# Performance work log

Hardware: AMD Instinct MI355X
Metric: run time of the kernel (lower is better)

Reference implementation:

```python
import jax, jax.numpy as jnp
import numpy as np

N = 200000  # num nodes == num edges (edge_weight serves as both node feature and edge weight)
D_HID = 128
D_OUT = 2


def setup_inputs() -> dict:
    key = jax.random.key(0)
    ks = jax.random.split(key, 5)
    edge_index = jax.random.randint(ks[0], (2, N), 0, N, dtype=jnp.int64)
    edge_weight = jax.random.uniform(ks[1], (N,), dtype=jnp.float32)
    # Glorot-ish init for GCNConv linear layers (bias=True by default in PyG)
    W1 = jax.random.normal(ks[2], (1, D_HID), dtype=jnp.float32) * (1.0 / np.sqrt(1))
    W2 = jax.random.normal(ks[3], (D_HID, D_HID), dtype=jnp.float32) * (1.0 / np.sqrt(D_HID))
    W3 = jax.random.normal(ks[4], (D_HID, D_OUT), dtype=jnp.float32) * (1.0 / np.sqrt(D_HID))
    b1 = jnp.zeros((D_HID,), dtype=jnp.float32)
    b2 = jnp.zeros((D_HID,), dtype=jnp.float32)
    b3 = jnp.zeros((D_OUT,), dtype=jnp.float32)
    return {"edge_index": edge_index, "edge_weight": edge_weight,
            "W1": W1, "b1": b1, "W2": W2, "b2": b2, "W3": W3, "b3": b3}


def reference(edge_index, edge_weight, W1, b1, W2, b2, W3, b3):
    n = edge_weight.shape[0]
    src, dst = edge_index[0], edge_index[1]
    # GCN symmetric normalization with self-loops (PyG gcn_norm, fill_value=1.0)
    loops = jnp.arange(n)
    src_f = jnp.concatenate([src, loops])            # [2N]
    dst_f = jnp.concatenate([dst, loops])            # [2N]
    w_f = jnp.concatenate([edge_weight, jnp.ones((n,), edge_weight.dtype)])
    deg = jax.ops.segment_sum(w_f, dst_f, num_segments=n)
    dinv = jnp.where(deg > 0, deg ** -0.5, 0.0)
    norm = dinv[src_f] * w_f * dinv[dst_f]           # [2N], identical for all layers

    def conv(x, W, b):
        h = x @ W                                    # linear transform first (out <= in path)
        msg = h[src_f] * norm[:, None]               # gather + edge scale
        return jax.ops.segment_sum(msg, dst_f, num_segments=n) + b  # scatter-add aggregate

    x = edge_weight[:, None]                         # node features = edge weights, [N,1]
    x = jax.nn.relu(conv(x, W1, b1))
    x = jax.nn.relu(conv(x, W2, b2))
    x = jax.nn.relu(conv(x, W3, b3))
    return jax.nn.log_softmax(x, axis=1)
```

## Files before the change

kernel.cpp:

```cpp
#include <hip/hip_runtime.h>

#define NN 200000
#define NE 200000
#define DH 128
#define CAP 16

typedef float f32x4 __attribute__((ext_vector_type(4)));
typedef _Float16 f16x8 __attribute__((ext_vector_type(8)));
#define AS1 __attribute__((address_space(1)))
#define AS3 __attribute__((address_space(3)))

__device__ __forceinline__ unsigned pack2h(float a, float b) {
  unsigned short ua = __builtin_bit_cast(unsigned short, (_Float16)a);
  unsigned short ub = __builtin_bit_cast(unsigned short, (_Float16)b);
  return (unsigned)ua | ((unsigned)ub << 16);
}
__device__ __forceinline__ float deg_of(int p) {
  return (float)(((unsigned)p) & 0x03FFFFFFu) * (1.0f / 1048576.0f) + 1.0f;
}
__device__ __forceinline__ int cnt_of(int p) { return (int)(((unsigned)p) >> 26); }

__global__ void k_build(const int* __restrict__ src, const int* __restrict__ dst,
                        const float* __restrict__ ew, int* __restrict__ pdeg,
                        int2* __restrict__ slot,
                        const float* __restrict__ W2, unsigned* __restrict__ w2g) {
  int tid = threadIdx.x;
  int e = blockIdx.x * 256 + tid;
  if (e < NE) {
    int d = dst[e];
    int sv = src[e];
    float w = ew[e];
    int addend = __float2int_rn(w * 1048576.0f) | (1 << 26);
    int old = atomicAdd(&pdeg[d], addend);
    int r = (int)(((unsigned)old) >> 26);
    if (r < CAP) slot[d * CAP + r] = make_int2(sv, __float_as_int(w));
  }
  if (blockIdx.x < 32) {
    int gid = blockIdx.x * 256 + tid;
    int fkc = gid >> 8, l = (gid >> 2) & 63, dd = gid & 3;
    int n = (fkc >> 2) * 16 + (l & 15);
    int dwp = (fkc & 3) * 16 + (l >> 4) * 4 + dd;
    w2g[gid] = pack2h(W2[(2 * dwp) * DH + n], W2[(2 * dwp + 1) * DH + n]);
  }
}

__global__ void k_nodes(const float* __restrict__ ew, const int* __restrict__ pdeg,
                        int2* __restrict__ slot, float* __restrict__ s) {
  int d = blockIdx.x * 256 + threadIdx.x;
  if (d >= NN) return;
  int p = pdeg[d];
  float dv = rsqrtf(deg_of(p));
  int cnt = min(cnt_of(p), CAP);
  float acc = 0.f;
  for (int j0 = 0; j0 < cnt; j0 += 4) {
    int2 sl[4];
    int sidx[4];
    bool v[4];
#pragma unroll
    for (int u = 0; u < 4; u++) {
      v[u] = (j0 + u) < cnt;
      sl[u] = slot[d * CAP + min(j0 + u, CAP - 1)];
      sidx[u] = v[u] ? sl[u].x : d;
    }
    float dg[4], we[4];
#pragma unroll
    for (int u = 0; u < 4; u++) { dg[u] = deg_of(pdeg[sidx[u]]); we[u] = ew[sidx[u]]; }
#pragma unroll
    for (int u = 0; u < 4; u++) {
      if (v[u]) {
        float wdvs = __int_as_float(sl[u].y) * rsqrtf(dg[u]);
        acc = fmaf(wdvs, we[u], acc);
        slot[d * CAP + j0 + u] = make_int2(sl[u].x, __float_as_int(wdvs * dv));
      }
    }
  }
  s[d] = dv * fmaf(dv, ew[d], acc);
}

__global__ __launch_bounds__(256, 3) void k_layer2(
    const float* __restrict__ s, const int* __restrict__ pdeg,
    const int2* __restrict__ slot,
    const float* __restrict__ W1, const float* __restrict__ b1,
    const float* __restrict__ b2, const float* __restrict__ W3,
    const unsigned* __restrict__ w2g, float* __restrict__ h3) {
  __shared__ __align__(16) char smem[49152];
  unsigned* w2t = (unsigned*)smem;
  uint4* tAf = (uint4*)(smem + 32768);
  float* eS = (float*)(smem + 32768);
  float* eN = (float*)(smem + 32768 + 4352);
  int tid = threadIdx.x;
  int wv = tid >> 6;

#pragma unroll
  for (int i = 0; i < 8; ++i)
    __builtin_amdgcn_global_load_lds(
        (const AS1 unsigned*)(w2g + i * 1024 + tid * 4),
        (AS3 unsigned*)(w2t + i * 1024 + wv * 256), 16, 0, 0);

  int base = blockIdx.x * 64;
  int lr15 = tid & 15, q = (tid >> 4) & 3;
  int d = base + wv * 16 + lr15;
  int myn = wv * 16 + lr15;

  int2 sl4[4];
#pragma unroll
  for (int it = 0; it < 4; ++it) sl4[it] = slot[base * CAP + it * 256 + tid];

  float w1r[32], b1r[32];
#pragma unroll
  for (int c = 0; c < 32; c++) { w1r[c] = W1[q * 32 + c]; b1r[c] = b1[q * 32 + c]; }
  int pd = pdeg[d];
  float sd = s[d];
  float dvd = rsqrtf(deg_of(pd));
  float sn = dvd * dvd;
  int mycnt = min(cnt_of(pd), CAP);

#pragma unroll
  for (int it = 0; it < 4; ++it) {
    int idx = it * 256 + tid;
    int nl = idx >> 4, j = idx & 15;
    if ((unsigned)sl4[it].x < NN) {
      eS[nl * 17 + j] = s[sl4[it].x];
      eN[nl * 17 + j] = __int_as_float(sl4[it].y);
    }
  }

  float acc[32];
#pragma unroll
  for (int c = 0; c < 32; c++)
    acc[c] = sn * fmaxf(fmaf(sd, w1r[c], b1r[c]), 0.f);
  __syncthreads();

  for (int j = 0; j < mycnt; ++j) {
    float ss = eS[myn * 17 + j], nr = eN[myn * 17 + j];
#pragma unroll
    for (int c = 0; c < 32; c++)
      acc[c] = fmaf(nr, fmaxf(fmaf(ss, w1r[c], b1r[c]), 0.f), acc[c]);
  }
  __syncthreads();

#pragma unroll
  for (int hi = 0; hi < 4; ++hi) {
    uint4 u;
    u.x = pack2h(acc[8 * hi + 0], acc[8 * hi + 1]);
    u.y = pack2h(acc[8 * hi + 2], acc[8 * hi + 3]);
    u.z = pack2h(acc[8 * hi + 4], acc[8 * hi + 5]);
    u.w = pack2h(acc[8 * hi + 6], acc[8 * hi + 7]);
    tAf[(wv * 4 + q) * 64 + hi * 16 + lr15] = u;
  }
  __syncthreads();

  int l = tid & 63, g = l >> 4, lr = l & 15;
  f32x4 acc8[8];
#pragma unroll
  for (int f = 0; f < 8; f++) acc8[f] = (f32x4){0.f, 0.f, 0.f, 0.f};
#pragma unroll
  for (int kc = 0; kc < 4; kc++) {
    f16x8 av = __builtin_bit_cast(f16x8, tAf[(wv * 4 + kc) * 64 + l]);
#pragma unroll
    for (int f = 0; f < 8; f++) {
      f16x8 bv = __builtin_bit_cast(f16x8, *(const uint4*)(w2t + ((f * 4 + kc) * 64 + l) * 4));
      acc8[f] = __builtin_amdgcn_mfma_f32_16x16x32_f16(av, bv, acc8[f], 0, 0, 0);
    }
  }

  float p0[4] = {0.f, 0.f, 0.f, 0.f}, p1[4] = {0.f, 0.f, 0.f, 0.f};
#pragma unroll
  for (int f = 0; f < 8; f++) {
    int n = f * 16 + lr;
    float bb = b2[n];
    float2 w3v = ((const float2*)W3)[n];
#pragma unroll
    for (int r = 0; r < 4; r++) {
      float v = fmaxf(acc8[f][r] + bb, 0.f);
      p0[r] = fmaf(v, w3v.x, p0[r]);
      p1[r] = fmaf(v, w3v.y, p1[r]);
    }
  }
#pragma unroll
  for (int r = 0; r < 4; r++) {
#pragma unroll
    for (int m = 8; m; m >>= 1) {
      p0[r] += __shfl_xor(p0[r], m);
      p1[r] += __shfl_xor(p1[r], m);
    }
  }
  if (lr == 0) {
#pragma unroll
    for (int r = 0; r < 4; r++) {
      int node = base + wv * 16 + g * 4 + r;
      ((float2*)h3)[node] = make_float2(p0[r], p1[r]);
    }
  }
}

__global__ void k_final(const float* __restrict__ h3, const int* __restrict__ pdeg,
                        const int2* __restrict__ slot, const float* __restrict__ b3,
                        float* __restrict__ out) {
  int d = blockIdx.x * 256 + threadIdx.x;
  if (d >= NN) return;
  int p = pdeg[d];
  float dvd = rsqrtf(deg_of(p));
  float sn = dvd * dvd;
  int cnt = min(cnt_of(p), CAP);
  float2 hv = ((const float2*)h3)[d];
  float y0 = sn * hv.x, y1 = sn * hv.y;
  for (int j0 = 0; j0 < cnt; j0 += 4) {
    int2 sl[4];
    int idx4[4];
    bool v[4];
#pragma unroll
    for (int u = 0; u < 4; u++) {
      v[u] = (j0 + u) < cnt;
      sl[u] = slot[d * CAP + min(j0 + u, CAP - 1)];
      idx4[u] = v[u] ? sl[u].x : d;
    }
    float2 hs[4];
#pragma unroll
    for (int u = 0; u < 4; u++) hs[u] = ((const float2*)h3)[idx4[u]];
#pragma unroll
    for (int u = 0; u < 4; u++) {
      if (v[u]) {
        float nr = __int_as_float(sl[u].y);
        y0 = fmaf(nr, hs[u].x, y0);
        y1 = fmaf(nr, hs[u].y, y1);
      }
    }
  }
  float z0 = fmaxf(y0 + b3[0], 0.f);
  float z1 = fmaxf(y1 + b3[1], 0.f);
  float m = fmaxf(z0, z1);
  float lse = m + logf(expf(z0 - m) + expf(z1 - m));
  out[2 * d] = z0 - lse;
  out[2 * d + 1] = z1 - lse;
}

extern "C" void kernel_launch(void* const* d_in, const int* in_sizes, int n_in,
                              void* d_out, int out_size, void* d_ws, size_t ws_size,
                              hipStream_t stream) {
  const int* ei = (const int*)d_in[0];
  const int* srcp = ei;
  const int* dstp = ei + NE;
  const float* ew = (const float*)d_in[1];
  const float* W1 = (const float*)d_in[2];
  const float* b1 = (const float*)d_in[3];
  const float* W2 = (const float*)d_in[4];
  const float* b2 = (const float*)d_in[5];
  const float* W3 = (const float*)d_in[6];
  const float* b3 = (const float*)d_in[7];
  float* out = (float*)d_out;

  char* ws = (char*)d_ws;
  size_t off = 0;
  auto alloc = [&](size_t bytes) -> void* {
    void* p = ws + off;
    off = (off + bytes + 255) & ~size_t(255);
    return p;
  };
  int* pdeg = (int*)alloc(NN * 4);
  size_t zero_bytes = off;
  int2* slot = (int2*)alloc((size_t)NN * CAP * 8);
  float* s = (float*)alloc(NN * 4);
  unsigned* w2g = (unsigned*)alloc(8192 * 4);
  float* h3 = (float*)alloc(NN * 2 * 4);
  (void)ws_size; (void)in_sizes; (void)n_in; (void)out_size;

  const int nbE = (NE + 255) / 256;
  const int nbN = (NN + 255) / 256;

  hipMemsetAsync(pdeg, 0, zero_bytes, stream);
  k_build<<<nbE, 256, 0, stream>>>(srcp, dstp, ew, pdeg, slot, W2, w2g);
  k_nodes<<<nbN, 256, 0, stream>>>(ew, pdeg, slot, s);
  k_layer2<<<NN / 64, 256, 0, stream>>>(s, pdeg, slot, W1, b1, b2, W3, w2g, h3);
  k_final<<<nbN, 256, 0, stream>>>(h3, pdeg, slot, b3, out);
}
```

Baseline: 132.1 us.

## Process two tiles per layer2 block and specialize neighbor loops for low degree

k_layer2 now runs half as many blocks, and each block handles two 64-node tiles. This amortizes the 32KB W2 LDS load and the W1/b1 register setup. The LDS neighbor staging is cut to 12 slots per node, and neighbors beyond 12 fall back to direct global loads. k_nodes and k_final load the first four slots with two 16-byte vector loads and handle the remaining neighbors in a scalar loop, avoiding the old padded min-clamped batch of four. The cost is fewer resident blocks in layer2, which gives less parallelism and latency hiding, plus extra syncs between tiles.

```diff
diff --git a/kernel.cpp b/kernel.cpp
--- a/kernel.cpp
+++ b/kernel.cpp
@@ -4,6 +4,8 @@
 #define NE 200000
 #define DH 128
 #define CAP 16
+#define NTILES (NN / 64)
+#define L2BLK ((NTILES + 1) / 2)
 
 typedef float f32x4 __attribute__((ext_vector_type(4)));
 typedef _Float16 f16x8 __attribute__((ext_vector_type(8)));
@@ -51,28 +53,31 @@
   int p = pdeg[d];
   float dv = rsqrtf(deg_of(p));
   int cnt = min(cnt_of(p), CAP);
+  const int4* sp = (const int4*)(slot + d * CAP);
+  int4 a = sp[0], b = sp[1];
+  int2 sl[4] = {{a.x, a.y}, {a.z, a.w}, {b.x, b.y}, {b.z, b.w}};
+  int n4 = min(cnt, 4);
+  int sidx[4];
+  bool v[4];
+#pragma unroll
+  for (int u = 0; u < 4; u++) { v[u] = u < n4; sidx[u] = v[u] ? sl[u].x : d; }
+  float dg[4], we[4];
+#pragma unroll
+  for (int u = 0; u < 4; u++) { dg[u] = deg_of(pdeg[sidx[u]]); we[u] = ew[sidx[u]]; }
   float acc = 0.f;
-  for (int j0 = 0; j0 < cnt; j0 += 4) {
-    int2 sl[4];
-    int sidx[4];
-    bool v[4];
-#pragma unroll
-    for (int u = 0; u < 4; u++) {
-      v[u] = (j0 + u) < cnt;
-      sl[u] = slot[d * CAP + min(j0 + u, CAP - 1)];
-      sidx[u] = v[u] ? sl[u].x : d;
-    }
-    float dg[4], we[4];
-#pragma unroll
-    for (int u = 0; u < 4; u++) { dg[u] = deg_of(pdeg[sidx[u]]); we[u] = ew[sidx[u]]; }
-#pragma unroll
-    for (int u = 0; u < 4; u++) {
-      if (v[u]) {
-        float wdvs = __int_as_float(sl[u].y) * rsqrtf(dg[u]);
-        acc = fmaf(wdvs, we[u], acc);
-        slot[d * CAP + j0 + u] = make_int2(sl[u].x, __float_as_int(wdvs * dv));
-      }
-    }
+#pragma unroll
+  for (int u = 0; u < 4; u++) {
+    if (v[u]) {
+      float wdvs = __int_as_float(sl[u].y) * rsqrtf(dg[u]);
+      acc = fmaf(wdvs, we[u], acc);
+      slot[d * CAP + u] = make_int2(sl[u].x, __float_as_int(wdvs * dv));
+    }
+  }
+  for (int j = 4; j < cnt; ++j) {
+    int2 t = slot[d * CAP + j];
+    float wdvs = __int_as_float(t.y) * rsqrtf(deg_of(pdeg[t.x]));
+    acc = fmaf(wdvs, ew[t.x], acc);
+    slot[d * CAP + j] = make_int2(t.x, __float_as_int(wdvs * dv));
   }
   s[d] = dv * fmaf(dv, ew[d], acc);
 }
@@ -87,7 +92,7 @@
   unsigned* w2t = (unsigned*)smem;
   uint4* tAf = (uint4*)(smem + 32768);
   float* eS = (float*)(smem + 32768);
-  float* eN = (float*)(smem + 32768 + 4352);
+  float* eN = (float*)(smem + 32768 + 3328);
   int tid = threadIdx.x;
   int wv = tid >> 6;
 
@@ -97,99 +102,119 @@
         (const AS1 unsigned*)(w2g + i * 1024 + tid * 4),
         (AS3 unsigned*)(w2t + i * 1024 + wv * 256), 16, 0, 0);
 
-  int base = blockIdx.x * 64;
   int lr15 = tid & 15, q = (tid >> 4) & 3;
-  int d = base + wv * 16 + lr15;
+  int l = tid & 63, g = l >> 4, lr = l & 15;
   int myn = wv * 16 + lr15;
-
-  int2 sl4[4];
-#pragma unroll
-  for (int it = 0; it < 4; ++it) sl4[it] = slot[base * CAP + it * 256 + tid];
-
   float w1r[32], b1r[32];
 #pragma unroll
   for (int c = 0; c < 32; c++) { w1r[c] = W1[q * 32 + c]; b1r[c] = b1[q * 32 + c]; }
-  int pd = pdeg[d];
-  float sd = s[d];
-  float dvd = rsqrtf(deg_of(pd));
-  float sn = dvd * dvd;
-  int mycnt = min(cnt_of(pd), CAP);
-
-#pragma unroll
-  for (int it = 0; it < 4; ++it) {
-    int idx = it * 256 + tid;
-    int nl = idx >> 4, j = idx & 15;
-    if ((unsigned)sl4[it].x < NN) {
-      eS[nl * 17 + j] = s[sl4[it].x];
-      eN[nl * 17 + j] = __int_as_float(sl4[it].y);
-    }
-  }
-
-  float acc[32];
-#pragma unroll
-  for (int c = 0; c < 32; c++)
-    acc[c] = sn * fmaxf(fmaf(sd, w1r[c], b1r[c]), 0.f);
-  __syncthreads();
-
-  for (int j = 0; j < mycnt; ++j) {
-    float ss = eS[myn * 17 + j], nr = eN[myn * 17 + j];
+
+  for (int t = 0; t < 2; ++t) {
+    int tile = blockIdx.x + t * L2BLK;
+    if (tile >= NTILES) break;
+    int base = tile * 64;
+    int d = base + myn;
+
+    int2 sl3[3];
+#pragma unroll
+    for (int it = 0; it < 3; ++it) {
+      int idx = it * 256 + tid;
+      int nl = idx / 12, j = idx - nl * 12;
+      sl3[it] = slot[base * CAP + nl * CAP + j];
+    }
+    int pd = pdeg[d];
+    float sd = s[d];
+    float dvd = rsqrtf(deg_of(pd));
+    float sn = dvd * dvd;
+    int mycnt = min(cnt_of(pd), CAP);
+
+    if (t > 0) __syncthreads();
+#pragma unroll
+    for (int it = 0; it < 3; ++it) {
+      int idx = it * 256 + tid;
+      int nl = idx / 12, j = idx - nl * 12;
+      if ((unsigned)sl3[it].x < NN) {
+        eS[nl * 13 + j] = s[sl3[it].x];
+        eN[nl * 13 + j] = __int_as_float(sl3[it].y);
+      }
+    }
+
+    float acc[32];
 #pragma unroll
     for (int c = 0; c < 32; c++)
-      acc[c] = fmaf(nr, fmaxf(fmaf(ss, w1r[c], b1r[c]), 0.f), acc[c]);
-  }
-  __syncthreads();
-
-#pragma unroll
-  for (int hi = 0; hi < 4; ++hi) {
-    uint4 u;
-    u.x = pack2h(acc[8 * hi + 0], acc[8 * hi + 1]);
-    u.y = pack2h(acc[8 * hi + 2], acc[8 * hi + 3]);
-    u.z = pack2h(acc[8 * hi + 4], acc[8 * hi + 5]);
-    u.w = pack2h(acc[8 * hi + 6], acc[8 * hi + 7]);
-    tAf[(wv * 4 + q) * 64 + hi * 16 + lr15] = u;
-  }
-  __syncthreads();
-
-  int l = tid & 63, g = l >> 4, lr = l & 15;
-  f32x4 acc8[8];
-#pragma unroll
-  for (int f = 0; f < 8; f++) acc8[f] = (f32x4){0.f, 0.f, 0.f, 0.f};
-#pragma unroll
-  for (int kc = 0; kc < 4; kc++) {
-    f16x8 av = __builtin_bit_cast(f16x8, tAf[(wv * 4 + kc) * 64 + l]);
+      acc[c] = sn * fmaxf(fmaf(sd, w1r[c], b1r[c]), 0.f);
+    __syncthreads();
+
+    int c12 = min(mycnt, 12);
+    for (int j = 0; j < c12; ++j) {
+      float ss = eS[myn * 13 + j], nr = eN[myn * 13 + j];
+#pragma unroll
+      for (int c = 0; c < 32; c++)
+        acc[c] = fmaf(nr, fmaxf(fmaf(ss, w1r[c], b1r[c]), 0.f), acc[c]);
+    }
+    if (mycnt > 12) {
+      for (int j = 12; j < mycnt; ++j) {
+        int2 sl = slot[d * CAP + j];
+        float ss = s[sl.x];
+        float nr = __int_as_float(sl.y);
+#pragma unroll
+        for (int c = 0; c < 32; c++)
+          acc[c] = fmaf(nr, fmaxf(fmaf(ss, w1r[c], b1r[c]), 0.f), acc[c]);
+      }
+    }
+    __syncthreads();
+
+#pragma unroll
+    for (int hi = 0; hi < 4; ++hi) {
+      uint4 u;
+      u.x = pack2h(acc[8 * hi + 0], acc[8 * hi + 1]);
+      u.y = pack2h(acc[8 * hi + 2], acc[8 * hi + 3]);
+      u.z = pack2h(acc[8 * hi + 4], acc[8 * hi + 5]);
+      u.w = pack2h(acc[8 * hi + 6], acc[8 * hi + 7]);
+      tAf[(wv * 4 + q) * 64 + hi * 16 + lr15] = u;
+    }
+    __syncthreads();
+
+    f32x4 acc8[8];
+#pragma unroll
+    for (int f = 0; f < 8; f++) acc8[f] = (f32x4){0.f, 0.f, 0.f, 0.f};
+#pragma unroll
+    for (int kc = 0; kc < 4; kc++) {
+      f16x8 av = __builtin_bit_cast(f16x8, tAf[(wv * 4 + kc) * 64 + l]);
+#pragma unroll
+      for (int f = 0; f < 8; f++) {
+        f16x8 bv = __builtin_bit_cast(f16x8, *(const uint4*)(w2t + ((f * 4 + kc) * 64 + l) * 4));
+        acc8[f] = __builtin_amdgcn_mfma_f32_16x16x32_f16(av, bv, acc8[f], 0, 0, 0);
+      }
+    }
+
+    float p0[4] = {0.f, 0.f, 0.f, 0.f}, p1[4] = {0.f, 0.f, 0.f, 0.f};
 #pragma unroll
     for (int f = 0; f < 8; f++) {
-      f16x8 bv = __builtin_bit_cast(f16x8, *(const uint4*)(w2t + ((f * 4 + kc) * 64 + l) * 4));
-      acc8[f] = __builtin_amdgcn_mfma_f32_16x16x32_f16(av, bv, acc8[f], 0, 0, 0);
-    }
-  }
-
-  float p0[4] = {0.f, 0.f, 0.f, 0.f}, p1[4] = {0.f, 0.f, 0.f, 0.f};
-#pragma unroll
-  for (int f = 0; f < 8; f++) {
-    int n = f * 16 + lr;
-    float bb = b2[n];
-    float2 w3v = ((const float2*)W3)[n];
+      int n = f * 16 + lr;
+      float bb = b2[n];
+      float2 w3v = ((const float2*)W3)[n];
+#pragma unroll
+      for (int r = 0; r < 4; r++) {
+        float v = fmaxf(acc8[f][r] + bb, 0.f);
+        p0[r] = fmaf(v, w3v.x, p0[r]);
+        p1[r] = fmaf(v, w3v.y, p1[r]);
+      }
+    }
 #pragma unroll
     for (int r = 0; r < 4; r++) {
-      float v = fmaxf(acc8[f][r] + bb, 0.f);
-      p0[r] = fmaf(v, w3v.x, p0[r]);
-      p1[r] = fmaf(v, w3v.y, p1[r]);
-    }
-  }
-#pragma unroll
-  for (int r = 0; r < 4; r++) {
-#pragma unroll
-    for (int m = 8; m; m >>= 1) {
-      p0[r] += __shfl_xor(p0[r], m);
-      p1[r] += __shfl_xor(p1[r], m);
-    }
-  }
-  if (lr == 0) {
-#pragma unroll
-    for (int r = 0; r < 4; r++) {
-      int node = base + wv * 16 + g * 4 + r;
-      ((float2*)h3)[node] = make_float2(p0[r], p1[r]);
+#pragma unroll
+      for (int m = 8; m; m >>= 1) {
+        p0[r] += __shfl_xor(p0[r], m);
+        p1[r] += __shfl_xor(p1[r], m);
+      }
+    }
+    if (lr == 0) {
+#pragma unroll
+      for (int r = 0; r < 4; r++) {
+        int node = base + wv * 16 + g * 4 + r;
+        ((float2*)h3)[node] = make_float2(p0[r], p1[r]);
+      }
     }
   }
 }
@@ -203,29 +228,33 @@
   float dvd = rsqrtf(deg_of(p));
   float sn = dvd * dvd;
   int cnt = min(cnt_of(p), CAP);
+  const int4* sp = (const int4*)(slot + d * CAP);
+  int4 a = sp[0], b = sp[1];
+  int2 sl[4] = {{a.x, a.y}, {a.z, a.w}, {b.x, b.y}, {b.z, b.w}};
   float2 hv = ((const float2*)h3)[d];
   float y0 = sn * hv.x, y1 = sn * hv.y;
-  for (int j0 = 0; j0 < cnt; j0 += 4) {
-    int2 sl[4];
-    int idx4[4];
-    bool v[4];
-#pragma unroll
-    for (int u = 0; u < 4; u++) {
-      v[u] = (j0 + u) < cnt;
-      sl[u] = slot[d * CAP + min(j0 + u, CAP - 1)];
-      idx4[u] = v[u] ? sl[u].x : d;
-    }
-    float2 hs[4];
-#pragma unroll
-    for (int u = 0; u < 4; u++) hs[u] = ((const float2*)h3)[idx4[u]];
-#pragma unroll
-    for (int u = 0; u < 4; u++) {
-      if (v[u]) {
-        float nr = __int_as_float(sl[u].y);
-        y0 = fmaf(nr, hs[u].x, y0);
-        y1 = fmaf(nr, hs[u].y, y1);
-      }
-    }
+  int n4 = min(cnt, 4);
+  int idx4[4];
+  bool v[4];
+#pragma unroll
+  for (int u = 0; u < 4; u++) { v[u] = u < n4; idx4[u] = v[u] ? sl[u].x : d; }
+  float2 hs[4];
+#pragma unroll
+  for (int u = 0; u < 4; u++) hs[u] = ((const float2*)h3)[idx4[u]];
+#pragma unroll
+  for (int u = 0; u < 4; u++) {
+    if (v[u]) {
+      float nr = __int_as_float(sl[u].y);
+      y0 = fmaf(nr, hs[u].x, y0);
+      y1 = fmaf(nr, hs[u].y, y1);
+    }
+  }
+  for (int j = 4; j < cnt; ++j) {
+    int2 t = slot[d * CAP + j];
+    float nr = __int_as_float(t.y);
+    float2 h = ((const float2*)h3)[t.x];
+    y0 = fmaf(nr, h.x, y0);
+    y1 = fmaf(nr, h.y, y1);
   }
   float z0 = fmaxf(y0 + b3[0], 0.f);
   float z1 = fmaxf(y1 + b3[1], 0.f);
@@ -271,6 +300,6 @@
   hipMemsetAsync(pdeg, 0, zero_bytes, stream);
   k_build<<<nbE, 256, 0, stream>>>(srcp, dstp, ew, pdeg, slot, W2, w2g);
   k_nodes<<<nbN, 256, 0, stream>>>(ew, pdeg, slot, s);
-  k_layer2<<<NN / 64, 256, 0, stream>>>(s, pdeg, slot, W1, b1, b2, W3, w2g, h3);
+  k_layer2<<<L2BLK, 256, 0, stream>>>(s, pdeg, slot, W1, b1, b2, W3, w2g, h3);
   k_final<<<nbN, 256, 0, stream>>>(h3, pdeg, slot, b3, out);
 }
```

Measured after the change: 131.7 us. No clear change (-0.3%).
